# Optimization experiments

Hardware: AMD Instinct MI355X
Metric: run time of the kernel (lower is better)

Reference implementation:

```python
import jax, jax.numpy as jnp
import numpy as np

NUM_HEADS = 16
SLICE_SIZE = 1024
SCALING = SLICE_SIZE ** 0.5  # module divides by sqrt(slice_size), as written


def setup_inputs() -> dict:
    key = jax.random.key(0)
    ks = jax.random.split(key, 9)
    B, S, D = 4, 2048, SLICE_SIZE
    sc = 0.02
    return {
        "x": jax.random.normal(ks[0], (B, S, D), dtype=jnp.float32),
        "Wq": jax.random.normal(ks[1], (D, D), dtype=jnp.float32) * sc,
        "bq": jax.random.normal(ks[2], (D,), dtype=jnp.float32) * sc,
        "Wk": jax.random.normal(ks[3], (D, D), dtype=jnp.float32) * sc,
        "bk": jax.random.normal(ks[4], (D,), dtype=jnp.float32) * sc,
        "Wv": jax.random.normal(ks[5], (D, D), dtype=jnp.float32) * sc,
        "bv": jax.random.normal(ks[6], (D,), dtype=jnp.float32) * sc,
        "Wp": jax.random.normal(ks[7], (D, D), dtype=jnp.float32) * sc,
        "bp": jax.random.normal(ks[8], (D,), dtype=jnp.float32) * sc,
    }


def _split_heads(t):
    # 'b s (h o) -> b h s o'
    b, s, d = t.shape
    return t.reshape(b, s, NUM_HEADS, d // NUM_HEADS).transpose(0, 2, 1, 3)


def reference(x, Wq, bq, Wk, bk, Wv, bv, Wp, bp):
    q = _split_heads(x @ Wq.T + bq)  # [B,H,S,O]
    k = _split_heads(x @ Wk.T + bk)
    v = _split_heads(x @ Wv.T + bv)
    energy = jnp.einsum('bhqo,bhko->bhqk', q, k)  # full score matrix
    attn = jax.nn.softmax(energy / SCALING, axis=-1)
    # Faithful to source: 'b h q k, b h v o -> b h v o' sums attn over (q,k)
    out = jnp.einsum('bhqk,bhvo->bhvo', attn, v)
    b, h, s, o = out.shape
    out = out.transpose(0, 2, 1, 3).reshape(b, s, h * o)  # 'b h v o -> b v (h o)'
    return out @ Wp.T + bp
```

## Files before the change

kernel.cpp:

```cpp
#include <hip/hip_runtime.h>
#include <cstdint>


typedef unsigned short u16;
typedef __bf16 bf16x8 __attribute__((ext_vector_type(8)));
typedef float f32x4 __attribute__((ext_vector_type(4)));

__device__ __forceinline__ u16 f2bf(float f) {
  unsigned int u = __float_as_uint(f);
  u += 0x7fffu + ((u >> 16) & 1u);
  return (u16)(u >> 16);
}

__device__ __forceinline__ void load16(const void* g, void* l) {
  auto gp = (const __attribute__((address_space(1))) unsigned int*)(uintptr_t)g;
  auto lp = (__attribute__((address_space(3))) unsigned int*)(unsigned int)(uintptr_t)l;
  __builtin_amdgcn_global_load_lds(gp, lp, 16, 0, 0);
}

__global__ void k_prep(const float* __restrict__ x, const float* __restrict__ Wv,
                       const float* __restrict__ bv, const float* __restrict__ Wp,
                       const float* __restrict__ bp, u16* __restrict__ xb,
                       u16* __restrict__ wpb, u16* __restrict__ wvtb,
                       float* __restrict__ cv) {
  __shared__ float tile[32][33];
  const int b = blockIdx.x;
  const int tid = threadIdx.x;
  if (b < 9216) {
    const float* src = (b < 8192) ? x : Wp;
    u16* dst = (b < 8192) ? xb : wpb;
    const long base = (long)((b < 8192) ? b : (b - 8192)) * 1024 + tid * 4;
    const float4 v = *(const float4*)(src + base);
    ushort4 o;
    o.x = f2bf(v.x); o.y = f2bf(v.y); o.z = f2bf(v.z); o.w = f2bf(v.w);
    *(ushort4*)(dst + base) = o;
  } else if (b < 10240) {
    const int tb = b - 9216;
    const int bi = (tb & 31) * 32;
    const int bj = (tb >> 5) * 32;
    const int tx = tid & 31;
    const int ty = tid >> 5;
    for (int r = ty; r < 32; r += 8)
      tile[r][tx] = Wv[(long)(bj + r) * 1024 + bi + tx];
    __syncthreads();
    for (int r = ty; r < 32; r += 8)
      wvtb[(long)(bi + r) * 1024 + bj + tx] = f2bf(tile[tx][r]);
  } else {
    const int row = (b - 10240) * 4 + (tid >> 6);
    const int lane = tid & 63;
    const float* w = Wp + (long)row * 1024;
    float s = 0.f;
    for (int j = lane; j < 1024; j += 64) s += w[j] * bv[j];
    for (int off = 32; off; off >>= 1) s += __shfl_down(s, off, 64);
    if (lane == 0) cv[row] = 2048.f * s + bp[row];
  }
}

__global__ void k_reduce(const float* __restrict__ p, u16* __restrict__ dst) {
  const long i = (long)(blockIdx.x * 256 + threadIdx.x) * 4;
  const float4 a = *(const float4*)(p + i);
  const float4 b = *(const float4*)(p + 1048576 + i);
  const float4 c = *(const float4*)(p + 2097152 + i);
  const float4 d = *(const float4*)(p + 3145728 + i);
  ushort4 o;
  o.x = f2bf((a.x + b.x + c.x + d.x) * 2048.f);
  o.y = f2bf((a.y + b.y + c.y + d.y) * 2048.f);
  o.z = f2bf((a.z + b.z + c.z + d.z) * 2048.f);
  o.w = f2bf((a.w + b.w + c.w + d.w) * 2048.f);
  *(ushort4*)(dst + i) = o;
}

template <int MODE>
__global__ __launch_bounds__(256) void k_gemm(
    const u16* __restrict__ A, const u16* __restrict__ B, float* __restrict__ Out,
    const float* __restrict__ bias, int M, int N, int K) {
  __shared__ u16 As[128 * 32];
  __shared__ u16 Bs[128 * 32];

  const int tid = threadIdx.x;
  const int lane = tid & 63;
  const int wv = tid >> 6;
  const int waveM = (wv & 1) << 6;
  const int waveN = (wv >> 1) << 6;
  const int l15 = lane & 15;
  const int quad = lane >> 4;

  long bm, bn;
  int kBeg, kEnd;
  if constexpr (MODE == 0) {
    const int id = blockIdx.x;
    const int xcd = id & 7;
    const int j = id >> 3;
    const int nb = N >> 7;
    const int mPerXcd = M / 128 / 8;
    bm = (long)(xcd * mPerXcd + j / nb) * 128;
    bn = (long)(j % nb) * 128;
    kBeg = 0; kEnd = K;
  } else {
    bm = (long)blockIdx.x * 128;
    bn = (long)blockIdx.y * 128;
    const int kChunk = K / gridDim.z;
    kBeg = blockIdx.z * kChunk;
    kEnd = kBeg + kChunk;
  }

  const int rl = lane >> 2;
  const int cs = (lane & 3) ^ ((lane >> 3) & 3);
  const u16* Ag0 = A + (bm + wv * 16 + rl) * (long)K + cs * 8;
  const u16* Bg0 = B + (bn + wv * 16 + rl) * (long)K + cs * 8;
  const long rowOff = 64 * (long)K;
  u16* Asl0 = As + wv * 512;
  u16* Asl1 = As + 2048 + wv * 512;
  u16* Bsl0 = Bs + wv * 512;
  u16* Bsl1 = Bs + 2048 + wv * 512;

  const f32x4 zero = {0.f, 0.f, 0.f, 0.f};
  f32x4 acc[4][4];
#pragma unroll
  for (int i = 0; i < 4; ++i)
#pragma unroll
    for (int j = 0; j < 4; ++j) acc[i][j] = zero;

  const int rq = quad ^ ((l15 >> 1) & 3);

  for (int k0 = kBeg; k0 < kEnd; k0 += 32) {
    __syncthreads();
    load16(Ag0 + k0, Asl0);
    load16(Ag0 + rowOff + k0, Asl1);
    load16(Bg0 + k0, Bsl0);
    load16(Bg0 + rowOff + k0, Bsl1);
    __syncthreads();

    bf16x8 af[4], bg[4];
#pragma unroll
    for (int t = 0; t < 4; ++t) {
      af[t] = *(const bf16x8*)(As + (waveM + t * 16 + l15) * 32 + rq * 8);
      bg[t] = *(const bf16x8*)(Bs + (waveN + t * 16 + l15) * 32 + rq * 8);
    }
#pragma unroll
    for (int i = 0; i < 4; ++i)
#pragma unroll
      for (int j = 0; j < 4; ++j)
        acc[i][j] = __builtin_amdgcn_mfma_f32_16x16x32_bf16(af[i], bg[j], acc[i][j], 0, 0, 0);
  }

  float* outp = (MODE == 1) ? Out + (long)blockIdx.z * M * N : Out;
#pragma unroll
  for (int i = 0; i < 4; ++i) {
    const long gm = bm + waveM + i * 16 + quad * 4;
#pragma unroll
    for (int j = 0; j < 4; ++j) {
      const long gn = bn + waveN + j * 16 + l15;
      const float bb = (MODE == 0) ? bias[gn] : 0.f;
#pragma unroll
      for (int r = 0; r < 4; ++r)
        outp[(gm + r) * N + gn] = acc[i][j][r] + bb;
    }
  }
}

extern "C" void kernel_launch(void* const* d_in, const int* in_sizes, int n_in,
                              void* d_out, int out_size, void* d_ws, size_t ws_size,
                              hipStream_t stream) {
  const float* x  = (const float*)d_in[0];
  const float* Wv = (const float*)d_in[5];
  const float* bv = (const float*)d_in[6];
  const float* Wp = (const float*)d_in[7];
  const float* bp = (const float*)d_in[8];

  char* ws = (char*)d_ws;
  u16* xb    = (u16*)(ws);
  u16* wpb   = (u16*)(ws + (16u << 20));
  u16* wvtb  = (u16*)(ws + (18u << 20));
  u16* m2b   = (u16*)(ws + (20u << 20));
  float* cv  = (float*)(ws + (22u << 20));
  float* m2f = (float*)(ws + (22u << 20) + 4096);

  k_prep<<<10496, 256, 0, stream>>>(x, Wv, bv, Wp, bp, xb, wpb, wvtb, cv);

  k_gemm<1><<<dim3(8, 8, 4), 256, 0, stream>>>(wpb, wvtb, m2f, nullptr,
                                               1024, 1024, 1024);
  k_reduce<<<1024, 256, 0, stream>>>(m2f, m2b);

  k_gemm<0><<<512, 256, 0, stream>>>(xb, m2b, (float*)d_out, cv,
                                     8192, 1024, 1024);
}
```

Before: 153.7 us.

## Triple-buffer LDS tiles in GEMM to overlap global loads with MFMA

Replaces the single-buffered load-then-compute GEMM loop with a three-stage LDS ring buffer. Tiles are prefetched two steps ahead with direct global-to-LDS loads, and completion is tracked with explicit vmcnt waits and raw barriers. The aim is to hide global memory latency behind MFMA work instead of stalling every K step. In exchange it triples LDS use per block, which may reduce occupancy, and its correctness depends on the hand-written vmcnt counts.

```diff
diff --git a/kernel.cpp b/kernel.cpp
--- a/kernel.cpp
+++ b/kernel.cpp
@@ -74,8 +74,8 @@
 __global__ __launch_bounds__(256) void k_gemm(
     const u16* __restrict__ A, const u16* __restrict__ B, float* __restrict__ Out,
     const float* __restrict__ bias, int M, int N, int K) {
-  __shared__ u16 As[128 * 32];
-  __shared__ u16 Bs[128 * 32];
+  __shared__ u16 As[3][128 * 32];
+  __shared__ u16 Bs[3][128 * 32];
 
   const int tid = threadIdx.x;
   const int lane = tid & 63;
@@ -109,10 +109,18 @@
   const u16* Ag0 = A + (bm + wv * 16 + rl) * (long)K + cs * 8;
   const u16* Bg0 = B + (bn + wv * 16 + rl) * (long)K + cs * 8;
   const long rowOff = 64 * (long)K;
-  u16* Asl0 = As + wv * 512;
-  u16* Asl1 = As + 2048 + wv * 512;
-  u16* Bsl0 = Bs + wv * 512;
-  u16* Bsl1 = Bs + 2048 + wv * 512;
+
+  const int nT = (kEnd - kBeg) >> 5;
+
+  auto STAGE = [&](int tt, int b) {
+    const long k0 = (long)kBeg + ((long)tt << 5);
+    u16* Ad = &As[b][0] + (wv << 9);
+    u16* Bd = &Bs[b][0] + (wv << 9);
+    load16(Ag0 + k0, Ad);
+    load16(Ag0 + rowOff + k0, Ad + 2048);
+    load16(Bg0 + k0, Bd);
+    load16(Bg0 + rowOff + k0, Bd + 2048);
+  };
 
   const f32x4 zero = {0.f, 0.f, 0.f, 0.f};
   f32x4 acc[4][4];
@@ -123,25 +131,38 @@
 
   const int rq = quad ^ ((l15 >> 1) & 3);
 
-  for (int k0 = kBeg; k0 < kEnd; k0 += 32) {
-    __syncthreads();
-    load16(Ag0 + k0, Asl0);
-    load16(Ag0 + rowOff + k0, Asl1);
-    load16(Bg0 + k0, Bsl0);
-    load16(Bg0 + rowOff + k0, Bsl1);
-    __syncthreads();
-
+  STAGE(0, 0);
+  if (nT > 1) STAGE(1, 1);
+
+  int cb = 0;
+  for (int tt = 0; tt < nT; ++tt) {
+    const int rem = nT - 1 - tt;
+    if (rem >= 2) {
+      STAGE(tt + 2, cb == 0 ? 2 : cb - 1);
+      asm volatile("s_waitcnt vmcnt(8)" ::: "memory");
+    } else if (rem == 1) {
+      asm volatile("s_waitcnt vmcnt(4)" ::: "memory");
+    } else {
+      asm volatile("s_waitcnt vmcnt(0)" ::: "memory");
+    }
+    __builtin_amdgcn_s_barrier();
+
+    const u16* Asb = &As[cb][0];
+    const u16* Bsb = &Bs[cb][0];
     bf16x8 af[4], bg[4];
 #pragma unroll
     for (int t = 0; t < 4; ++t) {
-      af[t] = *(const bf16x8*)(As + (waveM + t * 16 + l15) * 32 + rq * 8);
-      bg[t] = *(const bf16x8*)(Bs + (waveN + t * 16 + l15) * 32 + rq * 8);
+      af[t] = *(const bf16x8*)(Asb + (waveM + t * 16 + l15) * 32 + rq * 8);
+      bg[t] = *(const bf16x8*)(Bsb + (waveN + t * 16 + l15) * 32 + rq * 8);
     }
 #pragma unroll
     for (int i = 0; i < 4; ++i)
 #pragma unroll
       for (int j = 0; j < 4; ++j)
         acc[i][j] = __builtin_amdgcn_mfma_f32_16x16x32_bf16(af[i], bg[j], acc[i][j], 0, 0, 0);
+
+    __builtin_amdgcn_s_barrier();
+    cb = (cb == 2) ? 0 : cb + 1;
   }
 
   float* outp = (MODE == 1) ? Out + (long)blockIdx.z * M * N : Out;
```

Result: faster. 145.4 us (-5.4%).
